# Performance work log

Measured on AMD Instinct MI355X. Metric: run time of the kernel, lower is better.

The kernel has to match this reference:

```python
import jax, jax.numpy as jnp
import numpy as np

B, S, F, H = 64, 2048, 512, 512

def setup_inputs() -> dict:
    key = jax.random.key(0)
    ks = jax.random.split(key, 9)
    def xavier(k, shape):
        lim = float(np.sqrt(6.0 / (shape[0] + shape[1])))
        return jax.random.uniform(k, shape, jnp.float32, -lim, lim)
    inp = {"x": jax.random.normal(ks[0], (B, S, F), jnp.float32)}
    names = ["ii", "hi", "if_", "hf", "ig", "hg", "io", "ho"]
    for i, nm in enumerate(names):
        in_dim = F if nm[0] == "i" else H
        inp["w_" + nm] = xavier(ks[i + 1], (in_dim, H))
        inp["b_" + nm] = jnp.zeros((H,), jnp.float32)
    return inp

def reference(x, w_ii, b_ii, w_hi, b_hi, w_if_, b_if_, w_hf, b_hf,
              w_ig, b_ig, w_hg, b_hg, w_io, b_io, w_ho, b_ho):
    b = x.shape[0]
    h0 = jnp.zeros((b, w_hi.shape[0]), x.dtype)
    c0 = jnp.zeros_like(h0)
    # Precompute input projections for all timesteps (one big GEMM each):
    xi = jnp.einsum('bsf,fh->bsh', x, w_ii) + b_ii + b_hi  # fold both biases
    xf = jnp.einsum('bsf,fh->bsh', x, w_if_) + b_if_ + b_hf
    xg = jnp.einsum('bsf,fh->bsh', x, w_ig) + b_ig + b_hg
    xo = jnp.einsum('bsf,fh->bsh', x, w_io) + b_io + b_ho
    xs = jnp.stack([xi, xf, xg, xo], axis=0).transpose(2, 0, 1, 3)  # [S,4,B,H]

    def step(carry, x_t):
        h, c = carry
        i = jax.nn.sigmoid(x_t[0] + h @ w_hi)
        f = jax.nn.sigmoid(x_t[1] + h @ w_hf)
        g = jnp.tanh(x_t[2] + h @ w_hg)
        o = jax.nn.sigmoid(x_t[3] + h @ w_ho)
        c_new = f * c + i * g
        h_new = o * jnp.tanh(c_new)
        return (h_new, c_new), None

    (h_t, c_t), _ = jax.lax.scan(step, (h0, c0), xs)
    return (h_t, c_t)
```

## Files before the change

kernel.cpp:

```cpp
#include <hip/hip_runtime.h>

typedef unsigned short u16;
typedef unsigned int u32;
typedef unsigned long long u64;
typedef short short8 __attribute__((ext_vector_type(8)));
typedef float floatx4 __attribute__((ext_vector_type(4)));

#define SLEN 2048
#define BATCH 64
#define FDIM 512
#define HDIM 512
#define NWG 128
#define NTH 192
#define GROUPS 4
#define ROWS 16
#define HROW_U32 (HDIM/2)
#define HGRP_U32 (ROWS*HROW_U32)
#define HB_U32 (GROUPS*HGRP_U32)
#define WS_BYTES (4096 + 2*HB_U32*4)

#define LDS_W_U16 (4*16*64*8)
#define XR 20

__device__ __forceinline__ u16 f2bf_rne(float f) {
  union { float f; u32 u; } v; v.f = f;
  u32 u = v.u + 0x7FFFu + ((v.u >> 16) & 1u);
  return (u16)(u >> 16);
}
__device__ __forceinline__ float sigmoidf_fast(float x) {
  return 1.0f / (1.0f + __expf(-x));
}
__device__ __forceinline__ float tanhf_fast(float x) {
  return 1.0f - 2.0f / (__expf(2.0f * x) + 1.0f);
}

__device__ __forceinline__ void x_gemm2(
    const float* __restrict__ xrow, const u16* __restrict__ lds_wx,
    int g0, int lane, int n, int kq, float* __restrict__ sd)
{
  floatx4 a0 = {0.f, 0.f, 0.f, 0.f};
  floatx4 a1 = {0.f, 0.f, 0.f, 0.f};
#pragma unroll
  for (int kk = 0; kk < 16; ++kk) {
    floatx4 xa = *(const floatx4*)(xrow + kk*32 + kq*8);
    floatx4 xb = *(const floatx4*)(xrow + kk*32 + kq*8 + 4);
    short8 ax;
#pragma unroll
    for (int j = 0; j < 4; ++j) {
      ax[j]     = (short)f2bf_rne(xa[j]);
      ax[4 + j] = (short)f2bf_rne(xb[j]);
    }
    short8 b0 = *(const short8*)&lds_wx[(((g0    )*16 + kk)*64 + lane)*8];
    short8 b1 = *(const short8*)&lds_wx[(((g0 + 1)*16 + kk)*64 + lane)*8];
    a0 = __builtin_amdgcn_mfma_f32_16x16x32_bf16(ax, b0, a0, 0, 0, 0);
    a1 = __builtin_amdgcn_mfma_f32_16x16x32_bf16(ax, b1, a1, 0, 0, 0);
  }
  *(floatx4*)(sd + ((size_t)(g0    )*16 + n)*XR + kq*4) = a0;
  *(floatx4*)(sd + ((size_t)(g0 + 1)*16 + n)*XR + kq*4) = a1;
}

__global__ __launch_bounds__(NTH, 1)
void lstm_persistent(
    const float* __restrict__ x,
    const float* __restrict__ w_ii, const float* __restrict__ b_ii,
    const float* __restrict__ w_hi, const float* __restrict__ b_hi,
    const float* __restrict__ w_if, const float* __restrict__ b_if,
    const float* __restrict__ w_hf, const float* __restrict__ b_hf,
    const float* __restrict__ w_ig, const float* __restrict__ b_ig,
    const float* __restrict__ w_hg, const float* __restrict__ b_hg,
    const float* __restrict__ w_io, const float* __restrict__ b_io,
    const float* __restrict__ w_ho, const float* __restrict__ b_ho,
    float* __restrict__ out, u32* __restrict__ flags, u32* __restrict__ hbuf)
{
  __shared__ __align__(16) u16 lds_wh[LDS_W_U16];
  __shared__ __align__(16) u16 lds_wx[LDS_W_U16];
  __shared__ __align__(16) float scr_x[2][4][16][XR];

  const int tid  = threadIdx.x;
  const int g    = blockIdx.x & 3;
  const int c    = blockIdx.x >> 2;
  const int wv   = tid >> 6;
  const int lane = tid & 63;
  const int n    = lane & 15;
  const int kq   = lane >> 4;

  {
    const float* WH[4] = {w_hi, w_hf, w_hg, w_ho};
    const float* WX[4] = {w_ii, w_if, w_ig, w_io};
    for (int idx = tid; idx < 4*512*16; idx += NTH) {
      int col  = idx & 15;
      int k    = (idx >> 4) & 511;
      int gt   = idx >> 13;
      int kk   = k >> 5, rem = k & 31, quad = rem >> 3, j = rem & 7;
      int di   = ((gt*16 + kk)*64 + quad*16 + col)*8 + j;
      int src  = k*HDIM + c*16 + col;
      lds_wh[di] = f2bf_rne(WH[gt][src]);
      lds_wx[di] = f2bf_rne(WX[gt][src]);
    }
  }

  const int col = c*16 + n;
  const float bias0 = b_ii[col] + b_hi[col];
  const float bias1 = b_if[col] + b_hf[col];
  const float bias2 = b_ig[col] + b_hg[col];
  const float bias3 = b_io[col] + b_ho[col];
  floatx4 c_st = {0.f, 0.f, 0.f, 0.f};

  const float* xbase = x + (size_t)(g*ROWS + n) * (SLEN * FDIM);
  u32* flg = flags + (g << 5);

  __syncthreads();

  if (wv >= 1)
    x_gemm2(xbase, lds_wx, (wv - 1)*2, lane, n, kq, &scr_x[0][0][0][0]);

  for (int t = 0; t < SLEN; ++t) {
    __syncthreads();

    if (wv >= 1) {
      if (t + 1 < SLEN)
        x_gemm2(xbase + (size_t)(t + 1)*FDIM, lds_wx, (wv - 1)*2, lane, n, kq,
                &scr_x[(t + 1) & 1][0][0][0]);
    } else {
      const float* sx = &scr_x[t & 1][0][0][0];
      floatx4 sxv0 = *(const floatx4*)(sx + (0*16 + n)*XR + kq*4);
      floatx4 sxv1 = *(const floatx4*)(sx + (1*16 + n)*XR + kq*4);
      floatx4 sxv2 = *(const floatx4*)(sx + (2*16 + n)*XR + kq*4);
      floatx4 sxv3 = *(const floatx4*)(sx + (3*16 + n)*XR + kq*4);

      floatx4 acc0 = {0.f,0.f,0.f,0.f}, acc1 = {0.f,0.f,0.f,0.f};
      floatx4 acc2 = {0.f,0.f,0.f,0.f}, acc3 = {0.f,0.f,0.f,0.f};

      if (t > 0) {
        const u32* fp = flg + (lane & 31);
        while (__hip_atomic_load(fp, __ATOMIC_RELAXED, __HIP_MEMORY_SCOPE_AGENT) < (u32)t)
          __builtin_amdgcn_s_sleep(1);
        asm volatile("" ::: "memory");

        const u64* hrow = (const u64*)(hbuf + (t & 1)*HB_U32 + g*HGRP_U32 + n*HROW_U32);
        u64 hv[32];
#pragma unroll
        for (int kk = 0; kk < 16; ++kk) {
          hv[2*kk]   = __hip_atomic_load(&hrow[kk*8 + kq*2],     __ATOMIC_RELAXED, __HIP_MEMORY_SCOPE_AGENT);
          hv[2*kk+1] = __hip_atomic_load(&hrow[kk*8 + kq*2 + 1], __ATOMIC_RELAXED, __HIP_MEMORY_SCOPE_AGENT);
        }
#pragma unroll
        for (int kk = 0; kk < 16; ++kk) {
          union { u64 q[2]; short8 s; } ha;
          ha.q[0] = hv[2*kk]; ha.q[1] = hv[2*kk+1];
          acc0 = __builtin_amdgcn_mfma_f32_16x16x32_bf16(ha.s, *(const short8*)&lds_wh[((0*16+kk)*64+lane)*8], acc0, 0,0,0);
          acc1 = __builtin_amdgcn_mfma_f32_16x16x32_bf16(ha.s, *(const short8*)&lds_wh[((1*16+kk)*64+lane)*8], acc1, 0,0,0);
          acc2 = __builtin_amdgcn_mfma_f32_16x16x32_bf16(ha.s, *(const short8*)&lds_wh[((2*16+kk)*64+lane)*8], acc2, 0,0,0);
          acc3 = __builtin_amdgcn_mfma_f32_16x16x32_bf16(ha.s, *(const short8*)&lds_wh[((3*16+kk)*64+lane)*8], acc3, 0,0,0);
        }
      }

      float hnew[4];
#pragma unroll
      for (int r = 0; r < 4; ++r) {
        float gi = sigmoidf_fast(acc0[r] + sxv0[r] + bias0);
        float gf = sigmoidf_fast(acc1[r] + sxv1[r] + bias1);
        float gg = tanhf_fast  (acc2[r] + sxv2[r] + bias2);
        float go = sigmoidf_fast(acc3[r] + sxv3[r] + bias3);
        c_st[r] = gf * c_st[r] + gi * gg;
        hnew[r] = go * tanhf_fast(c_st[r]);
      }

      if (t == SLEN - 1) {
#pragma unroll
        for (int r = 0; r < 4; ++r) {
          int row = g*ROWS + kq*4 + r;
          out[row*HDIM + col]              = hnew[r];
          out[BATCH*HDIM + row*HDIM + col] = c_st[r];
        }
      } else {
        u32 hb[4];
#pragma unroll
        for (int r = 0; r < 4; ++r) hb[r] = (u32)f2bf_rne(hnew[r]);
        u32* hdst = hbuf + ((t + 1) & 1)*HB_U32 + g*HGRP_U32;
#pragma unroll
        for (int r = 0; r < 4; ++r) {
          u32 o = (u32)__shfl_xor((int)hb[r], 1);
          if ((n & 1) == 0) {
            u32 val = (o << 16) | hb[r];
            __hip_atomic_store(&hdst[(kq*4 + r)*HROW_U32 + c*8 + (n >> 1)],
                               val, __ATOMIC_RELAXED, __HIP_MEMORY_SCOPE_AGENT);
          }
        }
        asm volatile("s_waitcnt vmcnt(0)" ::: "memory");
        if (tid == 0)
          __hip_atomic_store(&flg[c], (u32)(t + 1), __ATOMIC_RELAXED,
                             __HIP_MEMORY_SCOPE_AGENT);
      }
    }
  }
}

extern "C" void kernel_launch(void* const* d_in, const int* in_sizes, int n_in,
                              void* d_out, int out_size, void* d_ws, size_t ws_size,
                              hipStream_t stream) {
  u32* flags = (u32*)d_ws;
  u32* hbuf  = (u32*)((char*)d_ws + 4096);
  (void)hipMemsetAsync(d_ws, 0, 4096, stream);

  lstm_persistent<<<dim3(NWG), dim3(NTH), 0, stream>>>(
      (const float*)d_in[0],
      (const float*)d_in[1],  (const float*)d_in[2],
      (const float*)d_in[3],  (const float*)d_in[4],
      (const float*)d_in[5],  (const float*)d_in[6],
      (const float*)d_in[7],  (const float*)d_in[8],
      (const float*)d_in[9],  (const float*)d_in[10],
      (const float*)d_in[11], (const float*)d_in[12],
      (const float*)d_in[13], (const float*)d_in[14],
      (const float*)d_in[15], (const float*)d_in[16],
      (float*)d_out, flags, hbuf);
}
```

Before: 9.168 ms.

## Replace flag barrier with sentinel-polled 4-slot h ring and per-gate x-projection waves

Drops the per-step flag counter and its store/load round trip. The recurrent wave now polls the h data itself with coherent vector loads until no word equals an all-ones sentinel, then resets the previous slot to the sentinel; this uses a 4-deep ring buffer initialised with a 0xFF memset. The input-projection work is split across four waves, one per gate, and prefetched two steps ahead so it stays off the recurrent critical path. This removes one global-memory latency hop per timestep, at the cost of spinning on full h reloads and relying on bf16 h values never equalling 0xFFFF pairs.

```diff
diff --git a/kernel.cpp b/kernel.cpp
--- a/kernel.cpp
+++ b/kernel.cpp
@@ -5,19 +5,22 @@
 typedef unsigned long long u64;
 typedef short short8 __attribute__((ext_vector_type(8)));
 typedef float floatx4 __attribute__((ext_vector_type(4)));
+typedef u32 u32x4 __attribute__((ext_vector_type(4)));
 
 #define SLEN 2048
 #define BATCH 64
 #define FDIM 512
 #define HDIM 512
 #define NWG 128
-#define NTH 192
+#define NTH 320
 #define GROUPS 4
 #define ROWS 16
 #define HROW_U32 (HDIM/2)
 #define HGRP_U32 (ROWS*HROW_U32)
 #define HB_U32 (GROUPS*HGRP_U32)
-#define WS_BYTES (4096 + 2*HB_U32*4)
+#define NRING 4
+#define WS_BYTES (NRING*HB_U32*4)
+#define SENT 0xFFFFFFFFu
 
 #define LDS_W_U16 (4*16*64*8)
 #define XR 20
@@ -34,12 +37,11 @@
   return 1.0f - 2.0f / (__expf(2.0f * x) + 1.0f);
 }
 
-__device__ __forceinline__ void x_gemm2(
+__device__ __forceinline__ void x_gemm1(
     const float* __restrict__ xrow, const u16* __restrict__ lds_wx,
-    int g0, int lane, int n, int kq, float* __restrict__ sd)
+    int gt, int lane, int n, int kq, float* __restrict__ sd)
 {
   floatx4 a0 = {0.f, 0.f, 0.f, 0.f};
-  floatx4 a1 = {0.f, 0.f, 0.f, 0.f};
 #pragma unroll
   for (int kk = 0; kk < 16; ++kk) {
     floatx4 xa = *(const floatx4*)(xrow + kk*32 + kq*8);
@@ -50,14 +52,15 @@
       ax[j]     = (short)f2bf_rne(xa[j]);
       ax[4 + j] = (short)f2bf_rne(xb[j]);
     }
-    short8 b0 = *(const short8*)&lds_wx[(((g0    )*16 + kk)*64 + lane)*8];
-    short8 b1 = *(const short8*)&lds_wx[(((g0 + 1)*16 + kk)*64 + lane)*8];
+    short8 b0 = *(const short8*)&lds_wx[((gt*16 + kk)*64 + lane)*8];
     a0 = __builtin_amdgcn_mfma_f32_16x16x32_bf16(ax, b0, a0, 0, 0, 0);
-    a1 = __builtin_amdgcn_mfma_f32_16x16x32_bf16(ax, b1, a1, 0, 0, 0);
-  }
-  *(floatx4*)(sd + ((size_t)(g0    )*16 + n)*XR + kq*4) = a0;
-  *(floatx4*)(sd + ((size_t)(g0 + 1)*16 + n)*XR + kq*4) = a1;
-}
+  }
+  *(floatx4*)(sd + ((size_t)gt*16 + n)*XR + kq*4) = a0;
+}
+
+#define HL(I, OFF) \
+  asm volatile("global_load_dwordx4 %0, %1, off offset:" OFF " sc0 sc1" \
+               : "=v"(hv[I]) : "v"(hp))
 
 __global__ __launch_bounds__(NTH, 1)
 void lstm_persistent(
@@ -70,11 +73,11 @@
     const float* __restrict__ w_hg, const float* __restrict__ b_hg,
     const float* __restrict__ w_io, const float* __restrict__ b_io,
     const float* __restrict__ w_ho, const float* __restrict__ b_ho,
-    float* __restrict__ out, u32* __restrict__ flags, u32* __restrict__ hbuf)
+    float* __restrict__ out, u32* __restrict__ hbuf)
 {
   __shared__ __align__(16) u16 lds_wh[LDS_W_U16];
   __shared__ __align__(16) u16 lds_wx[LDS_W_U16];
-  __shared__ __align__(16) float scr_x[2][4][16][XR];
+  __shared__ __align__(16) float scr_x[4][4][16][XR];
 
   const int tid  = threadIdx.x;
   const int g    = blockIdx.x & 3;
@@ -107,22 +110,23 @@
   floatx4 c_st = {0.f, 0.f, 0.f, 0.f};
 
   const float* xbase = x + (size_t)(g*ROWS + n) * (SLEN * FDIM);
-  u32* flg = flags + (g << 5);
 
   __syncthreads();
 
-  if (wv >= 1)
-    x_gemm2(xbase, lds_wx, (wv - 1)*2, lane, n, kq, &scr_x[0][0][0][0]);
+  if (wv >= 1) {
+    x_gemm1(xbase,        lds_wx, wv - 1, lane, n, kq, &scr_x[0][0][0][0]);
+    x_gemm1(xbase + FDIM, lds_wx, wv - 1, lane, n, kq, &scr_x[1][0][0][0]);
+  }
 
   for (int t = 0; t < SLEN; ++t) {
     __syncthreads();
 
     if (wv >= 1) {
-      if (t + 1 < SLEN)
-        x_gemm2(xbase + (size_t)(t + 1)*FDIM, lds_wx, (wv - 1)*2, lane, n, kq,
-                &scr_x[(t + 1) & 1][0][0][0]);
+      if (t + 2 < SLEN)
+        x_gemm1(xbase + (size_t)(t + 2)*FDIM, lds_wx, wv - 1, lane, n, kq,
+                &scr_x[(t + 2) & 3][0][0][0]);
     } else {
-      const float* sx = &scr_x[t & 1][0][0][0];
+      const float* sx = &scr_x[t & 3][0][0][0];
       floatx4 sxv0 = *(const floatx4*)(sx + (0*16 + n)*XR + kq*4);
       floatx4 sxv1 = *(const floatx4*)(sx + (1*16 + n)*XR + kq*4);
       floatx4 sxv2 = *(const floatx4*)(sx + (2*16 + n)*XR + kq*4);
@@ -132,22 +136,40 @@
       floatx4 acc2 = {0.f,0.f,0.f,0.f}, acc3 = {0.f,0.f,0.f,0.f};
 
       if (t > 0) {
-        const u32* fp = flg + (lane & 31);
-        while (__hip_atomic_load(fp, __ATOMIC_RELAXED, __HIP_MEMORY_SCOPE_AGENT) < (u32)t)
-          __builtin_amdgcn_s_sleep(1);
-        asm volatile("" ::: "memory");
-
-        const u64* hrow = (const u64*)(hbuf + (t & 1)*HB_U32 + g*HGRP_U32 + n*HROW_U32);
-        u64 hv[32];
+        const u32* hp = hbuf + (size_t)(t & 3)*HB_U32 + g*HGRP_U32 + n*HROW_U32 + kq*4;
+        u32x4 hv[16];
+        int ready;
+        do {
+          HL(0,"0");   HL(1,"64");  HL(2,"128"); HL(3,"192");
+          HL(4,"256"); HL(5,"320"); HL(6,"384"); HL(7,"448");
+          HL(8,"512"); HL(9,"576"); HL(10,"640"); HL(11,"704");
+          HL(12,"768"); HL(13,"832"); HL(14,"896"); HL(15,"960");
+          asm volatile("s_waitcnt vmcnt(0)" ::: "memory");
+          __builtin_amdgcn_sched_barrier(0);
+          u32 mx = 0u;
+#pragma unroll
+          for (int i = 0; i < 16; ++i) {
+#pragma unroll
+            for (int j = 0; j < 4; ++j) {
+              u32 w = hv[i][j];
+              mx = (w > mx) ? w : mx;
+            }
+          }
+          ready = __all((int)(mx != SENT));
+        } while (!ready);
+
+        {
+          u32* rz = hbuf + (size_t)((t - 1) & 3)*HB_U32 + g*HGRP_U32;
+          int i0 = lane, i1 = lane + 64;
+          __hip_atomic_store(&rz[(i0 >> 3)*HROW_U32 + c*8 + (i0 & 7)], SENT,
+                             __ATOMIC_RELAXED, __HIP_MEMORY_SCOPE_AGENT);
+          __hip_atomic_store(&rz[(i1 >> 3)*HROW_U32 + c*8 + (i1 & 7)], SENT,
+                             __ATOMIC_RELAXED, __HIP_MEMORY_SCOPE_AGENT);
+        }
+
 #pragma unroll
         for (int kk = 0; kk < 16; ++kk) {
-          hv[2*kk]   = __hip_atomic_load(&hrow[kk*8 + kq*2],     __ATOMIC_RELAXED, __HIP_MEMORY_SCOPE_AGENT);
-          hv[2*kk+1] = __hip_atomic_load(&hrow[kk*8 + kq*2 + 1], __ATOMIC_RELAXED, __HIP_MEMORY_SCOPE_AGENT);
-        }
-#pragma unroll
-        for (int kk = 0; kk < 16; ++kk) {
-          union { u64 q[2]; short8 s; } ha;
-          ha.q[0] = hv[2*kk]; ha.q[1] = hv[2*kk+1];
+          union { u32x4 u; short8 s; } ha; ha.u = hv[kk];
           acc0 = __builtin_amdgcn_mfma_f32_16x16x32_bf16(ha.s, *(const short8*)&lds_wh[((0*16+kk)*64+lane)*8], acc0, 0,0,0);
           acc1 = __builtin_amdgcn_mfma_f32_16x16x32_bf16(ha.s, *(const short8*)&lds_wh[((1*16+kk)*64+lane)*8], acc1, 0,0,0);
           acc2 = __builtin_amdgcn_mfma_f32_16x16x32_bf16(ha.s, *(const short8*)&lds_wh[((2*16+kk)*64+lane)*8], acc2, 0,0,0);
@@ -177,7 +199,7 @@
         u32 hb[4];
 #pragma unroll
         for (int r = 0; r < 4; ++r) hb[r] = (u32)f2bf_rne(hnew[r]);
-        u32* hdst = hbuf + ((t + 1) & 1)*HB_U32 + g*HGRP_U32;
+        u32* hdst = hbuf + (size_t)((t + 1) & 3)*HB_U32 + g*HGRP_U32;
 #pragma unroll
         for (int r = 0; r < 4; ++r) {
           u32 o = (u32)__shfl_xor((int)hb[r], 1);
@@ -187,10 +209,6 @@
                                val, __ATOMIC_RELAXED, __HIP_MEMORY_SCOPE_AGENT);
           }
         }
-        asm volatile("s_waitcnt vmcnt(0)" ::: "memory");
-        if (tid == 0)
-          __hip_atomic_store(&flg[c], (u32)(t + 1), __ATOMIC_RELAXED,
-                             __HIP_MEMORY_SCOPE_AGENT);
       }
     }
   }
@@ -199,9 +217,8 @@
 extern "C" void kernel_launch(void* const* d_in, const int* in_sizes, int n_in,
                               void* d_out, int out_size, void* d_ws, size_t ws_size,
                               hipStream_t stream) {
-  u32* flags = (u32*)d_ws;
-  u32* hbuf  = (u32*)((char*)d_ws + 4096);
-  (void)hipMemsetAsync(d_ws, 0, 4096, stream);
+  u32* hbuf = (u32*)d_ws;
+  (void)hipMemsetAsync(d_ws, 0xFF, WS_BYTES, stream);
 
   lstm_persistent<<<dim3(NWG), dim3(NTH), 0, stream>>>(
       (const float*)d_in[0],
@@ -213,5 +230,5 @@
       (const float*)d_in[11], (const float*)d_in[12],
       (const float*)d_in[13], (const float*)d_in[14],
       (const float*)d_in[15], (const float*)d_in[16],
-      (float*)d_out, flags, hbuf);
-}
+      (float*)d_out, hbuf);
+}
```

Measured after the change: 9.909 ms. 8.1% more time.
